# Optimization experiments

Measured on AMD Instinct MI355X. Metric: run time of the kernel, lower is better.

## Reference

```python
import jax, jax.numpy as jnp
import numpy as np

B, N, F_IN = 32, 1024, 128
H1, H2, OUT = 64, 32, 10
EDGE_P = 0.01  # edge probability for random adjacency


def setup_inputs() -> dict:
    key = jax.random.key(0)
    ks = jax.random.split(key, 16)
    x = jax.random.normal(ks[0], (B, N, F_IN), dtype=jnp.float32)
    # dense binary adjacency per graph (module consumes dense [N,N] adj)
    adj = (jax.random.uniform(ks[1], (B, N, N)) < EDGE_P).astype(jnp.float32)
    mask = jnp.ones((B, N, 1), dtype=jnp.float32)
    s = 0.05
    W1a = jax.random.normal(ks[2], (F_IN, H1), dtype=jnp.float32) * s
    b1a = jnp.zeros((H1,), dtype=jnp.float32)
    W2a = jax.random.normal(ks[3], (H1, H1), dtype=jnp.float32) * s
    b2a = jnp.zeros((H1,), dtype=jnp.float32)
    W1b = jax.random.normal(ks[4], (H1, H2), dtype=jnp.float32) * s
    b1b = jnp.zeros((H2,), dtype=jnp.float32)
    W2b = jax.random.normal(ks[5], (H2, H2), dtype=jnp.float32) * s
    b2b = jnp.zeros((H2,), dtype=jnp.float32)
    Wfc = jax.random.normal(ks[6], (H2, OUT), dtype=jnp.float32) * s
    bfc = jnp.zeros((OUT,), dtype=jnp.float32)
    return dict(x=x, adj=adj, mask=mask, W1a=W1a, b1a=b1a, W2a=W2a, b2a=b2a,
                W1b=W1b, b1b=b1b, W2b=W2b, b2b=b2b, Wfc=Wfc, bfc=bfc)


def _gin_layer(h, adj, mask, Wa, ba, Wb, bb, eps=0.0):
    # neighbor sum aggregation: neigh[b,i] = sum_j adj[b,i,j] * h[b,j]
    neigh = jnp.einsum('bij,bjf->bif', adj, h)
    z = (1.0 + eps) * h + neigh
    z = jax.nn.relu(z @ Wa + ba) @ Wb + bb  # 2-layer MLP
    return z * mask  # zero out padded nodes


def reference(x, adj, mask, W1a, b1a, W2a, b2a, W1b, b1b, W2b, b2b, Wfc, bfc):
    h = _gin_layer(x, adj, mask, W1a, b1a, W2a, b2a)   # [B,N,64]
    h = _gin_layer(h, adj, mask, W1b, b1b, W2b, b2b)   # [B,N,32]
    g = jnp.max(h, axis=1)                              # graph readout [B,32]
    return g @ Wfc + bfc                                # [B,OUT] (dropout = eval identity)
```

## Files before the change

### kernel.cpp

```cpp
#include <hip/hip_runtime.h>
#include <cstdint>
#include <cstddef>


#define CAP 32

typedef float v4f __attribute__((ext_vector_type(4)));

__device__ __forceinline__ float rl(float x, int l) {
  return __int_as_float(__builtin_amdgcn_readlane(__float_as_int(x), l));
}

__global__ __launch_bounds__(256) void k_scanproj(
    const float* __restrict__ x, const float* __restrict__ W1a,
    float* __restrict__ u,
    const float* __restrict__ adj, int* __restrict__ nbr,
    int* __restrict__ deg) {
  int lane = threadIdx.x & 63;
  int wid  = threadIdx.x >> 6;
  if (blockIdx.x < 1024) {
    int p = blockIdx.x;
    int xcd = p & 7, q = p >> 3;
    int b = xcd + 8 * (q & 3);
    int chunk = q >> 2;
    int row0 = b * 1024 + chunk * 32 + wid * 8;
    row0 = __builtin_amdgcn_readfirstlane(row0);
    const float* xr = x + (size_t)row0 * 128;
    float acc[8] = {0, 0, 0, 0, 0, 0, 0, 0};
    for (int kc = 0; kc < 32; ++kc) {
      v4f xv[8];
      #pragma unroll
      for (int r = 0; r < 8; ++r)
        xv[r] = *(const v4f*)(xr + r * 128 + kc * 4);
      #pragma unroll
      for (int j = 0; j < 4; ++j) {
        float w = W1a[(kc * 4 + j) * 64 + lane];
        #pragma unroll
        for (int r = 0; r < 8; ++r)
          acc[r] = fmaf(xv[r][j], w, acc[r]);
      }
    }
    #pragma unroll
    for (int r = 0; r < 8; ++r)
      u[(size_t)(row0 + r) * 64 + lane] = acc[r];
  } else {
    int s = blockIdx.x - 1024;
    int xcd = s & 7, q = s >> 3;
    int b = xcd + 8 * (q & 3);
    int chunk = q >> 2;
    int node = b * 1024 + chunk * 4 + wid;
    const v4f* arow = (const v4f*)(adj + (size_t)node * 1024);
    int* outp = nbr + node * CAP;
    v4f a[4];
    #pragma unroll
    for (int c = 0; c < 4; ++c)
      a[c] = __builtin_nontemporal_load(arow + c * 64 + lane);
    int cnt = 0;
    #pragma unroll
    for (int c = 0; c < 4; ++c) {
      #pragma unroll
      for (int comp = 0; comp < 4; ++comp) {
        bool hit = (a[c][comp] != 0.0f);
        unsigned long long m = __ballot(hit);
        if (hit) {
          int below = __builtin_amdgcn_mbcnt_hi(
              (unsigned)(m >> 32),
              __builtin_amdgcn_mbcnt_lo((unsigned)m, 0));
          int pos = cnt + below;
          if (pos < CAP) outp[pos] = ((c * 64 + lane) << 2) + comp;
        }
        cnt += __popcll(m);
      }
    }
    if (lane == 0) deg[node] = cnt < CAP ? cnt : CAP;
  }
}

__global__ __launch_bounds__(256) void k_gathA(
    const float* __restrict__ u, const int* __restrict__ nbr,
    const int* __restrict__ deg, const float* __restrict__ mask,
    const float* __restrict__ b1a, const float* __restrict__ W2a,
    const float* __restrict__ b2a, const float* __restrict__ W1b,
    float* __restrict__ v) {
  __shared__ float sW2[64 * 64];
  __shared__ float sW1b[64 * 32];
  for (int t = threadIdx.x; t < 64 * 64; t += 256) sW2[t] = W2a[t];
  for (int t = threadIdx.x; t < 64 * 32; t += 256) sW1b[t] = W1b[t];
  __syncthreads();
  int lane = threadIdx.x & 63;
  int f = lane & 31, hh = lane >> 5;
  float ba1 = b1a[lane], ba2 = b2a[lane];
  int i = blockIdx.x, wid = threadIdx.x >> 6;
  int xcd = i & 7, j = i >> 3;
  int b = xcd + 8 * (j & 3);
  int w = j >> 2;
  int n0 = b * 1024 + w * 8 + wid * 2, n1 = n0 + 1;
  const float* ub = u + (size_t)b * 1024 * 64;
  int d0 = deg[n0], d1 = deg[n1];
  int nl = nbr[n0 * CAP + lane];
  float s0[8] = {0,0,0,0,0,0,0,0}, s1[8] = {0,0,0,0,0,0,0,0};
  int dmax = d0 > d1 ? d0 : d1;
  int rounds = (dmax + 7) >> 3;
  for (int rr = 0; rr < rounds; ++rr) {
    int base = rr << 3;
    #pragma unroll
    for (int i2 = 0; i2 < 8; ++i2) {
      int t = base + i2;
      int j0 = __builtin_amdgcn_readlane(nl, t);
      int j1 = __builtin_amdgcn_readlane(nl, 32 + t);
      bool ok0 = t < d0, ok1 = t < d1;
      j0 = ok0 ? j0 : 0;  j1 = ok1 ? j1 : 0;
      float v0 = ub[j0 * 64 + lane];
      float v1 = ub[j1 * 64 + lane];
      s0[i2] += ok0 ? v0 : 0.0f;
      s1[i2] += ok1 ? v1 : 0.0f;
    }
  }
  float acc0 = ub[(n0 & 1023) * 64 + lane]
             + (((s0[0]+s0[1])+(s0[2]+s0[3]))+((s0[4]+s0[5])+(s0[6]+s0[7])));
  float acc1 = ub[(n1 & 1023) * 64 + lane]
             + (((s1[0]+s1[1])+(s1[2]+s1[3]))+((s1[4]+s1[5])+(s1[6]+s1[7])));
  float r0 = fmaxf(acc0 + ba1, 0.0f);
  float r1 = fmaxf(acc1 + ba1, 0.0f);
  float a0=0,a1=0,a2=0,a3=0, c0=0,c1=0,c2=0,c3=0;
  #pragma unroll
  for (int k = 0; k < 64; k += 4) {
    float w0 = sW2[(k    ) * 64 + lane];
    float w1 = sW2[(k + 1) * 64 + lane];
    float w2 = sW2[(k + 2) * 64 + lane];
    float w3 = sW2[(k + 3) * 64 + lane];
    a0 = fmaf(rl(r0, k    ), w0, a0);  c0 = fmaf(rl(r1, k    ), w0, c0);
    a1 = fmaf(rl(r0, k + 1), w1, a1);  c1 = fmaf(rl(r1, k + 1), w1, c1);
    a2 = fmaf(rl(r0, k + 2), w2, a2);  c2 = fmaf(rl(r1, k + 2), w2, c2);
    a3 = fmaf(rl(r0, k + 3), w3, a3);  c3 = fmaf(rl(r1, k + 3), w3, c3);
  }
  float h20 = (ba2 + ((a0 + a1) + (a2 + a3))) * mask[n0];
  float h21 = (ba2 + ((c0 + c1) + (c2 + c3))) * mask[n1];
  float p00=0,p01=0, p10=0,p11=0;
  #pragma unroll
  for (int k0 = 0; k0 < 32; k0 += 2) {
    float w0 = sW1b[(hh * 32 + k0    ) * 32 + f];
    float w1 = sW1b[(hh * 32 + k0 + 1) * 32 + f];
    p00 = fmaf(__shfl(h20, hh * 32 + k0    ), w0, p00);
    p01 = fmaf(__shfl(h20, hh * 32 + k0 + 1), w1, p01);
    p10 = fmaf(__shfl(h21, hh * 32 + k0    ), w0, p10);
    p11 = fmaf(__shfl(h21, hh * 32 + k0 + 1), w1, p11);
  }
  float vp0 = p00 + p01;  vp0 += __shfl_xor(vp0, 32);
  float vp1 = p10 + p11;  vp1 += __shfl_xor(vp1, 32);
  if (hh == 0) {
    v[n0 * 32 + f] = vp0;
    v[n1 * 32 + f] = vp1;
  }
}

__global__ __launch_bounds__(256) void k_gathB(
    const float* __restrict__ v, const int* __restrict__ nbr,
    const int* __restrict__ deg, const float* __restrict__ mask,
    const float* __restrict__ b1b, const float* __restrict__ W2b,
    const float* __restrict__ b2b, float* __restrict__ pmax) {
  __shared__ float sW2b[32 * 32];
  __shared__ float wred[4][32];
  for (int t = threadIdx.x; t < 32 * 32; t += 256) sW2b[t] = W2b[t];
  __syncthreads();
  int lane = threadIdx.x & 63;
  int f = lane & 31, hh = lane >> 5;
  float bb1 = b1b[f], bb2 = b2b[f];
  int i = blockIdx.x, wid = threadIdx.x >> 6;
  int xcd = i & 7, j = i >> 3;
  int b = xcd + 8 * (j & 3);
  int w = j >> 2;
  int n0 = b * 1024 + w * 8 + wid * 2, n1 = n0 + 1;
  const float* vb = v + (size_t)b * 1024 * 32;
  int d0 = deg[n0], d1 = deg[n1];
  int nl = nbr[n0 * CAP + lane];
  float s0[8] = {0,0,0,0,0,0,0,0}, s1[8] = {0,0,0,0,0,0,0,0};
  int dmax = d0 > d1 ? d0 : d1;
  int rounds = (dmax + 15) >> 4;
  for (int rr = 0; rr < rounds; ++rr) {
    int base = rr << 4;
    #pragma unroll
    for (int i2 = 0; i2 < 8; ++i2) {
      int t = base + (i2 << 1) + hh;
      int j0 = __shfl(nl, t);
      int j1 = __shfl(nl, 32 + t);
      bool ok0 = t < d0, ok1 = t < d1;
      j0 = ok0 ? j0 : 0;  j1 = ok1 ? j1 : 0;
      float v0 = vb[j0 * 32 + f];
      float v1 = vb[j1 * 32 + f];
      s0[i2] += ok0 ? v0 : 0.0f;
      s1[i2] += ok1 ? v1 : 0.0f;
    }
  }
  float acc0 = ((s0[0]+s0[1])+(s0[2]+s0[3]))+((s0[4]+s0[5])+(s0[6]+s0[7]));
  float acc1 = ((s1[0]+s1[1])+(s1[2]+s1[3]))+((s1[4]+s1[5])+(s1[6]+s1[7]));
  acc0 += __shfl_xor(acc0, 32);
  acc1 += __shfl_xor(acc1, 32);
  float r0 = fmaxf(vb[(n0 & 1023) * 32 + f] + acc0 + bb1, 0.0f);
  float r1 = fmaxf(vb[(n1 & 1023) * 32 + f] + acc1 + bb1, 0.0f);
  float a0=0,a1=0,a2=0,a3=0, c0=0,c1=0,c2=0,c3=0;
  #pragma unroll
  for (int k = 0; k < 32; k += 4) {
    float w0 = sW2b[(k    ) * 32 + f];
    float w1 = sW2b[(k + 1) * 32 + f];
    float w2 = sW2b[(k + 2) * 32 + f];
    float w3 = sW2b[(k + 3) * 32 + f];
    a0 = fmaf(rl(r0, k    ), w0, a0);  c0 = fmaf(rl(r1, k    ), w0, c0);
    a1 = fmaf(rl(r0, k + 1), w1, a1);  c1 = fmaf(rl(r1, k + 1), w1, c1);
    a2 = fmaf(rl(r0, k + 2), w2, a2);  c2 = fmaf(rl(r1, k + 2), w2, c2);
    a3 = fmaf(rl(r0, k + 3), w3, a3);  c3 = fmaf(rl(r1, k + 3), w3, c3);
  }
  float o0 = (bb2 + ((a0 + a1) + (a2 + a3))) * mask[n0];
  float o1 = (bb2 + ((c0 + c1) + (c2 + c3))) * mask[n1];
  float m = fmaxf(o0, o1);
  if (hh == 0) wred[wid][f] = m;
  __syncthreads();
  if (threadIdx.x < 32) {
    float mm = fmaxf(fmaxf(wred[0][threadIdx.x], wred[1][threadIdx.x]),
                     fmaxf(wred[2][threadIdx.x], wred[3][threadIdx.x]));
    pmax[((b << 7) + w) * 32 + threadIdx.x] = mm;
  }
}

__global__ __launch_bounds__(1024) void k_fin(
    const float* __restrict__ pmax, const float* __restrict__ Wfc,
    const float* __restrict__ bfc, float* __restrict__ out) {
  __shared__ float red[32][33];
  __shared__ float g[32];
  int b = blockIdx.x;
  int f = threadIdx.x & 31, c = threadIdx.x >> 5;
  const float* pb = pmax + (size_t)b * 128 * 32;
  float m = -3.4e38f;
  #pragma unroll
  for (int q = 0; q < 4; ++q)
    m = fmaxf(m, pb[(c * 4 + q) * 32 + f]);
  red[c][f] = m;
  __syncthreads();
  if (c == 0) {
    float mm = red[0][f];
    #pragma unroll
    for (int k = 1; k < 32; ++k) mm = fmaxf(mm, red[k][f]);
    g[f] = mm;
  }
  __syncthreads();
  if (threadIdx.x < 10) {
    float o = bfc[threadIdx.x];
    #pragma unroll
    for (int k = 0; k < 32; ++k)
      o = fmaf(g[k], Wfc[k * 10 + threadIdx.x], o);
    out[b * 10 + threadIdx.x] = o;
  }
}

extern "C" void kernel_launch(void* const* d_in, const int* in_sizes, int n_in,
                              void* d_out, int out_size, void* d_ws, size_t ws_size,
                              hipStream_t stream) {
  const float* x    = (const float*)d_in[0];
  const float* adj  = (const float*)d_in[1];
  const float* mask = (const float*)d_in[2];
  const float* W1a  = (const float*)d_in[3];
  const float* b1a  = (const float*)d_in[4];
  const float* W2a  = (const float*)d_in[5];
  const float* b2a  = (const float*)d_in[6];
  const float* W1b  = (const float*)d_in[7];
  const float* b1b  = (const float*)d_in[8];
  const float* W2b  = (const float*)d_in[9];
  const float* b2b  = (const float*)d_in[10];
  const float* Wfc  = (const float*)d_in[11];
  const float* bfc  = (const float*)d_in[12];
  float* out = (float*)d_out;

  char* ws = (char*)d_ws;
  float* u    = (float*)(ws);
  float* v    = (float*)(ws + (8u << 20));
  int*   nbr  = (int*)  (ws + (12u << 20));
  int*   deg  = (int*)  (ws + (16u << 20));
  float* pmax = (float*)(ws + (21u << 20));

  hipLaunchKernelGGL(k_scanproj, dim3(9216), dim3(256), 0, stream,
                     x, W1a, u, adj, nbr, deg);
  hipLaunchKernelGGL(k_gathA,    dim3(4096), dim3(256), 0, stream,
                     u, nbr, deg, mask, b1a, W2a, b2a, W1b, v);
  hipLaunchKernelGGL(k_gathB,    dim3(4096), dim3(256), 0, stream,
                     v, nbr, deg, mask, b1b, W2b, b2b, pmax);
  hipLaunchKernelGGL(k_fin,      dim3(32),   dim3(1024), 0, stream,
                     pmax, Wfc, bfc, out);
}
```

Before: 278.8 us.

## Scan two adjacency rows per wave and fully unroll neighbor gather loops

The adjacency scan path now has each wave process two rows, loading eight vectors up front. This halves the scan block count and switches the loads from nontemporal to regular. The gather loops in both aggregation kernels are fully unrolled to the CAP bound, with per-element predication replacing the degree-dependent trip count, so more loads can be in flight. Launch bounds now request occupancy of 4 blocks. The trade-off is more predicated-off loads of row 0 for low-degree nodes and higher register pressure in the scan.

Result: no change. 283.7 us (+1.7%).

```diff
diff --git a/kernel.cpp b/kernel.cpp
--- a/kernel.cpp
+++ b/kernel.cpp
@@ -48,35 +48,39 @@
     int xcd = s & 7, q = s >> 3;
     int b = xcd + 8 * (q & 3);
     int chunk = q >> 2;
-    int node = b * 1024 + chunk * 4 + wid;
-    const v4f* arow = (const v4f*)(adj + (size_t)node * 1024);
-    int* outp = nbr + node * CAP;
-    v4f a[4];
-    #pragma unroll
-    for (int c = 0; c < 4; ++c)
-      a[c] = __builtin_nontemporal_load(arow + c * 64 + lane);
-    int cnt = 0;
-    #pragma unroll
-    for (int c = 0; c < 4; ++c) {
+    int node0 = b * 1024 + chunk * 8 + wid * 2;
+    const v4f* arow = (const v4f*)(adj + (size_t)node0 * 1024);
+    v4f a[8];
+    #pragma unroll
+    for (int c = 0; c < 8; ++c)
+      a[c] = arow[c * 64 + lane];
+    #pragma unroll
+    for (int rrow = 0; rrow < 2; ++rrow) {
+      int node = node0 + rrow;
+      int* outp = nbr + node * CAP;
+      int cnt = 0;
       #pragma unroll
-      for (int comp = 0; comp < 4; ++comp) {
-        bool hit = (a[c][comp] != 0.0f);
-        unsigned long long m = __ballot(hit);
-        if (hit) {
-          int below = __builtin_amdgcn_mbcnt_hi(
-              (unsigned)(m >> 32),
-              __builtin_amdgcn_mbcnt_lo((unsigned)m, 0));
-          int pos = cnt + below;
-          if (pos < CAP) outp[pos] = ((c * 64 + lane) << 2) + comp;
+      for (int c = 0; c < 4; ++c) {
+        #pragma unroll
+        for (int comp = 0; comp < 4; ++comp) {
+          bool hit = (a[rrow * 4 + c][comp] != 0.0f);
+          unsigned long long m = __ballot(hit);
+          if (hit) {
+            int below = __builtin_amdgcn_mbcnt_hi(
+                (unsigned)(m >> 32),
+                __builtin_amdgcn_mbcnt_lo((unsigned)m, 0));
+            int pos = cnt + below;
+            if (pos < CAP) outp[pos] = ((c * 64 + lane) << 2) + comp;
+          }
+          cnt += __popcll(m);
         }
-        cnt += __popcll(m);
       }
-    }
-    if (lane == 0) deg[node] = cnt < CAP ? cnt : CAP;
-  }
-}
-
-__global__ __launch_bounds__(256) void k_gathA(
+      if (lane == 0) deg[node] = cnt < CAP ? cnt : CAP;
+    }
+  }
+}
+
+__global__ __launch_bounds__(256, 4) void k_gathA(
     const float* __restrict__ u, const int* __restrict__ nbr,
     const int* __restrict__ deg, const float* __restrict__ mask,
     const float* __restrict__ b1a, const float* __restrict__ W2a,
@@ -99,13 +103,11 @@
   int d0 = deg[n0], d1 = deg[n1];
   int nl = nbr[n0 * CAP + lane];
   float s0[8] = {0,0,0,0,0,0,0,0}, s1[8] = {0,0,0,0,0,0,0,0};
-  int dmax = d0 > d1 ? d0 : d1;
-  int rounds = (dmax + 7) >> 3;
-  for (int rr = 0; rr < rounds; ++rr) {
-    int base = rr << 3;
+  #pragma unroll
+  for (int r = 0; r < 4; ++r) {
     #pragma unroll
     for (int i2 = 0; i2 < 8; ++i2) {
-      int t = base + i2;
+      int t = r * 8 + i2;
       int j0 = __builtin_amdgcn_readlane(nl, t);
       int j1 = __builtin_amdgcn_readlane(nl, 32 + t);
       bool ok0 = t < d0, ok1 = t < d1;
@@ -154,7 +156,7 @@
   }
 }
 
-__global__ __launch_bounds__(256) void k_gathB(
+__global__ __launch_bounds__(256, 4) void k_gathB(
     const float* __restrict__ v, const int* __restrict__ nbr,
     const int* __restrict__ deg, const float* __restrict__ mask,
     const float* __restrict__ b1b, const float* __restrict__ W2b,
@@ -175,13 +177,11 @@
   int d0 = deg[n0], d1 = deg[n1];
   int nl = nbr[n0 * CAP + lane];
   float s0[8] = {0,0,0,0,0,0,0,0}, s1[8] = {0,0,0,0,0,0,0,0};
-  int dmax = d0 > d1 ? d0 : d1;
-  int rounds = (dmax + 15) >> 4;
-  for (int rr = 0; rr < rounds; ++rr) {
-    int base = rr << 4;
+  #pragma unroll
+  for (int r = 0; r < 2; ++r) {
     #pragma unroll
     for (int i2 = 0; i2 < 8; ++i2) {
-      int t = base + (i2 << 1) + hh;
+      int t = r * 16 + (i2 << 1) + hh;
       int j0 = __shfl(nl, t);
       int j1 = __shfl(nl, 32 + t);
       bool ok0 = t < d0, ok1 = t < d1;
@@ -277,7 +277,7 @@
   int*   deg  = (int*)  (ws + (16u << 20));
   float* pmax = (float*)(ws + (21u << 20));
 
-  hipLaunchKernelGGL(k_scanproj, dim3(9216), dim3(256), 0, stream,
+  hipLaunchKernelGGL(k_scanproj, dim3(5120), dim3(256), 0, stream,
                      x, W1a, u, adj, nbr, deg);
   hipLaunchKernelGGL(k_gathA,    dim3(4096), dim3(256), 0, stream,
                      u, nbr, deg, mask, b1a, W2a, b2a, W1b, v);
```
